# Optimization experiments

Measured on AMD Instinct MI355X. Metric: run time of the kernel, lower is better.

The kernel has to match this reference:

```python
import jax, jax.numpy as jnp
import numpy as np

B, N, C, H, NC, P = 16, 577, 768, 12, 8, 576  # batch, seq(=patches+cls), dim, heads, curves, patches
D = C // H


def setup_inputs() -> dict:
    key = jax.random.key(0)
    ks = jax.random.split(key, 8)
    x = jax.random.normal(ks[0], (B, N, C), jnp.float32)
    qkv_w = jax.random.normal(ks[1], (C, 3 * C), jnp.float32) * 0.02
    proj_w = jax.random.normal(ks[2], (C, C), jnp.float32) * 0.02
    proj_b = jnp.zeros((C,), jnp.float32)
    # learned per-head decay logits; +3 so sigmoid ~0.95 (slow decay, realistic)
    ai_list = jax.random.normal(ks[3], (NC, H), jnp.float32) + 3.0
    mask_weights = jax.random.normal(ks[4], (NC,), jnp.float32) * 0.1 + 1.0 / NC
    normalize = 1.0 + 0.1 * jax.random.normal(ks[5], (H,), jnp.float32)
    # space-filling-curve inverse index permutations (one per curve)
    curve_inds = jnp.stack([
        jax.random.permutation(jax.random.fold_in(ks[6], c), P) for c in range(NC)
    ]).astype(jnp.int32)
    return dict(x=x, qkv_w=qkv_w, proj_w=proj_w, proj_b=proj_b,
                ai_list=ai_list, mask_weights=mask_weights,
                normalize=normalize, curve_inds=curve_inds)


def _build_mask(ai_list, mask_weights, curve_inds):
    # sigmoid(a)^|i-j| gathered by the curve permutation == sigmoid(a)^|ind_i - ind_j|
    a = jax.nn.sigmoid(ai_list)                                  # [NC,H]
    ci = curve_inds.astype(jnp.float32)                          # [NC,P]
    diff = jnp.abs(ci[:, :, None] - ci[:, None, :])              # [NC,P,P]
    Mc = a[:, :, None, None] ** diff[:, None, :, :]              # [NC,H,P,P]
    Mp = jnp.einsum('c,chpq->hpq', mask_weights, Mc)             # weighted sum over curves
    # cls-token row/col: each curve contributes ones -> sum of weights
    sw = jnp.sum(mask_weights)
    M = jnp.pad(Mp, ((0, 0), (1, 0), (1, 0)))                    # [H,N,N]
    M = M.at[:, 0, :].set(sw)
    M = M.at[:, :, 0].set(sw)
    return M


def reference(x, qkv_w, proj_w, proj_b, ai_list, mask_weights, normalize, curve_inds):
    qkv = (x @ qkv_w).reshape(B, N, 3, H, D)
    q = jnp.transpose(qkv[:, :, 0], (0, 2, 1, 3))                # [B,H,N,D]
    k = jnp.transpose(qkv[:, :, 1], (0, 2, 1, 3))
    v = jnp.transpose(qkv[:, :, 2], (0, 2, 1, 3))
    # NOTE: original overwrites self.scale with the bool `scale`=True -> multiply by 1
    attn = jnp.einsum('bhnd,bhmd->bhnm', q, k)                   # [B,H,N,N]
    M = _build_mask(ai_list, mask_weights, curve_inds)           # [H,N,N]
    attn = attn * M[None] * normalize[None, :, None, None]       # method='mul_v1'
    attn = jax.nn.softmax(attn, axis=-1)
    out = jnp.einsum('bhnm,bhmd->bhnd', attn, v)
    out = jnp.transpose(out, (0, 2, 1, 3)).reshape(B, N, C)
    return out @ proj_w + proj_b
```

## Files before the change

kernel.cpp:

```cpp
#include <hip/hip_runtime.h>


typedef _Float16 f16;
typedef _Float16 half8 __attribute__((ext_vector_type(8)));
typedef _Float16 half4 __attribute__((ext_vector_type(4)));
typedef float floatx4 __attribute__((ext_vector_type(4)));

#define DEVINL __device__ __forceinline__

#define Bb 16
#define NN 577
#define CC 768
#define HH 12
#define DD 64
#define MM (Bb * NN)
#define VTLD 584
#define MLD 580
#define CLD 136

DEVINL void async_copy16(void* lds, const void* g) {
  __builtin_amdgcn_global_load_lds(
      (const __attribute__((address_space(1))) void*)g,
      (__attribute__((address_space(3))) void*)lds, 16, 0, 0);
}

DEVINL half8 ld_swz(const f16* lds, int row, int chunk) {
  return *(const half8*)(lds + row * 64 + ((chunk ^ (row & 7)) << 3));
}

DEVINL int xcd_swizzle(int orig, int nwg) {
  int q = nwg >> 3, r = nwg & 7;
  int xcd = orig & 7, loc = orig >> 3;
  return (xcd < r ? xcd * (q + 1) : r * (q + 1) + (xcd - r) * q) + loc;
}

__global__ void cvt_kernel(const float* __restrict__ in, f16* __restrict__ out, int n) {
  int i = (blockIdx.x * blockDim.x + threadIdx.x) * 4;
  if (i >= n) return;
  float4 v = *(const float4*)(in + i);
  half4 o = {(f16)v.x, (f16)v.y, (f16)v.z, (f16)v.w};
  *(half4*)(out + i) = o;
}

__global__ void transpose_cvt(const float* __restrict__ in, f16* __restrict__ out,
                              int N3, int K) {
  __shared__ float t[32][33];
  const int k0 = blockIdx.x * 32, n0 = blockIdx.y * 32;
  const int tx = threadIdx.x & 31, ty = threadIdx.x >> 5;
#pragma unroll
  for (int p = 0; p < 4; ++p)
    t[ty + p * 8][tx] = in[(size_t)(k0 + ty + p * 8) * N3 + n0 + tx];
  __syncthreads();
#pragma unroll
  for (int p = 0; p < 4; ++p)
    out[(size_t)(n0 + ty + p * 8) * K + k0 + tx] = (f16)t[tx][ty + p * 8];
}

__global__ void mask_kernel(const float* __restrict__ ai, const float* __restrict__ mw,
                            const float* __restrict__ nrm, const int* __restrict__ ci,
                            float* __restrict__ Mb) {
  const int i = blockIdx.x;
  const int h = blockIdx.y;
  __shared__ float la_s[8], wv_s[8], cif[8], swn_s;
  int tid = threadIdx.x;
  if (tid < 8) {
    float av = ai[tid * 12 + h];
    float a = 1.f / (1.f + __expf(-av));
    la_s[tid] = __logf(a);
    wv_s[tid] = mw[tid];
    cif[tid] = (i > 0) ? (float)ci[tid * 576 + (i - 1)] : 0.f;
  }
  if (tid == 0) {
    float s = 0.f;
    for (int c = 0; c < 8; ++c) s += mw[c];
    swn_s = s * nrm[h] * 1.44269504088896f;
  }
  __syncthreads();
  const float nr = nrm[h] * 1.44269504088896f;
  float* row = Mb + ((size_t)h * NN + i) * MLD;
  for (int j = tid; j < NN; j += blockDim.x) {
    float val;
    if (i == 0 || j == 0) {
      val = swn_s;
    } else {
      float acc = 0.f;
#pragma unroll
      for (int c = 0; c < 8; ++c) {
        float d = fabsf(cif[c] - (float)ci[c * 576 + (j - 1)]);
        acc += wv_s[c] * __expf(la_s[c] * d);
      }
      val = acc * nr;
    }
    row[j] = val;
  }
}

DEVINL void gemm_mainloop(const f16* __restrict__ A, const f16* __restrict__ Bt,
                          int K, int lda, int ldb, int arow0, int brow0, int maxar,
                          f16* As, f16* Bs, floatx4 acc[4][4], int tid) {
  const int lane = tid & 63;
  const int wid = tid >> 6;
  const int wr = wid >> 1, wc = wid & 1;
  const int l15 = lane & 15, g = lane >> 4;
  for (int k0 = 0; k0 < K; k0 += 64) {
#pragma unroll
    for (int q = 0; q < 4; ++q) {
      int idx = q * 256 + tid;
      int r = idx >> 3, cp = idx & 7;
      int lc = (cp ^ (r & 7)) << 3;
      int ar = arow0 + r; if (ar > maxar) ar = maxar;
      async_copy16(As + idx * 8, A + (size_t)ar * lda + k0 + lc);
      async_copy16(Bs + idx * 8, Bt + (size_t)(brow0 + r) * ldb + k0 + lc);
    }
    __syncthreads();
#pragma unroll
    for (int kk = 0; kk < 2; ++kk) {
      half8 af[4], bf[4];
#pragma unroll
      for (int mi = 0; mi < 4; ++mi) af[mi] = ld_swz(As, wr * 64 + mi * 16 + l15, kk * 4 + g);
#pragma unroll
      for (int ni = 0; ni < 4; ++ni) bf[ni] = ld_swz(Bs, wc * 64 + ni * 16 + l15, kk * 4 + g);
#pragma unroll
      for (int mi = 0; mi < 4; ++mi)
#pragma unroll
        for (int ni = 0; ni < 4; ++ni)
          acc[mi][ni] = __builtin_amdgcn_mfma_f32_16x16x32_f16(af[mi], bf[ni], acc[mi][ni], 0, 0, 0);
    }
    __syncthreads();
  }
}

__global__ __launch_bounds__(256, 3)
void gemm_qkv(const f16* __restrict__ A, const f16* __restrict__ Bt,
              f16* __restrict__ qb, f16* __restrict__ kb, f16* __restrict__ vt) {
  __shared__ __align__(16) f16 SMEM[128 * CLD];
  f16* As = SMEM;
  f16* Bs = SMEM + 8192;
  floatx4 acc[4][4] = {};
  const int nwg = 18 * 73;
  const int wgid = xcd_swizzle(blockIdx.y * gridDim.x + blockIdx.x, nwg);
  const int m0 = (wgid / 18) * 128, n0 = (wgid % 18) * 128;
  gemm_mainloop(A, Bt, CC, CC, CC, m0, n0, MM - 1, As, Bs, acc, threadIdx.x);
  const int tid = threadIdx.x, lane = tid & 63, wid = tid >> 6;
  const int wr = wid >> 1, wc = wid & 1, l15 = lane & 15, g = lane >> 4;
  const int t = n0 / CC;
  const int h0 = (n0 - t * CC) >> 6;
  if (t < 2) {
#pragma unroll
    for (int mi = 0; mi < 4; ++mi)
#pragma unroll
      for (int ni = 0; ni < 4; ++ni)
#pragma unroll
        for (int r = 0; r < 4; ++r)
          SMEM[(wr * 64 + mi * 16 + 4 * g + r) * CLD + wc * 64 + ni * 16 + l15] =
              (f16)acc[mi][ni][r];
    __syncthreads();
    f16* dst = (t == 0) ? qb : kb;
#pragma unroll
    for (int p = 0; p < 8; ++p) {
      int c = p * 256 + tid;
      int ml = c >> 4, n3c = (c & 15) << 3;
      int mg = m0 + ml;
      if (mg < MM) {
        int b = mg / NN, n = mg - b * NN;
        int h = h0 + (n3c >> 6), d0 = n3c & 63;
        half8 v = *(const half8*)(SMEM + ml * CLD + n3c);
        *(half8*)(dst + ((size_t)(b * HH + h) * NN + n) * DD + d0) = v;
      }
    }
  } else {
#pragma unroll
    for (int mi = 0; mi < 4; ++mi)
#pragma unroll
      for (int ni = 0; ni < 4; ++ni)
#pragma unroll
        for (int r = 0; r < 4; ++r)
          SMEM[(wc * 64 + ni * 16 + l15) * CLD + wr * 64 + mi * 16 + 4 * g + r] =
              (f16)acc[mi][ni][r];
    __syncthreads();
#pragma unroll
    for (int p = 0; p < 8; ++p) {
      int c = p * 256 + tid;
      int n3 = c >> 4, mc = (c & 15) << 3;
      int mg = m0 + mc;
      int h = h0 + (n3 >> 6), d = n3 & 63;
      half8 v = *(const half8*)(SMEM + n3 * CLD + mc);
      int b0 = mg / NN, b7 = (mg + 7) / NN;
      if (mg + 7 < MM && b0 == b7) {
        *(half8*)(vt + ((size_t)(b0 * HH + h) * DD + d) * VTLD + (mg - b0 * NN)) = v;
      } else {
#pragma unroll
        for (int e = 0; e < 8; ++e) {
          int m2 = mg + e;
          if (m2 < MM) {
            int b = m2 / NN;
            vt[((size_t)(b * HH + h) * DD + d) * VTLD + (m2 - b * NN)] = v[e];
          }
        }
      }
    }
  }
}

__global__ __launch_bounds__(256, 3)
void gemm_proj(const f16* __restrict__ A, const f16* __restrict__ Bt,
               const float* __restrict__ bias, float* __restrict__ out) {
  __shared__ f16 As[128 * 64], Bs[128 * 64];
  floatx4 acc[4][4] = {};
  const int nwg = 6 * 73;
  const int wgid = xcd_swizzle(blockIdx.y * gridDim.x + blockIdx.x, nwg);
  const int m0 = (wgid / 6) * 128, n0 = (wgid % 6) * 128;
  gemm_mainloop(A, Bt, CC, CC, CC, m0, n0, MM - 1, As, Bs, acc, threadIdx.x);
  const int lane = threadIdx.x & 63, wid = threadIdx.x >> 6;
  const int wr = wid >> 1, wc = wid & 1, l15 = lane & 15, g = lane >> 4;
#pragma unroll
  for (int mi = 0; mi < 4; ++mi)
#pragma unroll
    for (int ni = 0; ni < 4; ++ni)
#pragma unroll
      for (int r = 0; r < 4; ++r) {
        int m = m0 + wr * 64 + mi * 16 + 4 * g + r;
        if (m >= MM) continue;
        int n = n0 + wc * 64 + ni * 16 + l15;
        out[(size_t)m * CC + n] = acc[mi][ni][r] + bias[n];
      }
}

__global__ __launch_bounds__(256, 2)
void attn_kernel(const f16* __restrict__ qb, const f16* __restrict__ kb,
                 const f16* __restrict__ vt, const float* __restrict__ Mb,
                 f16* __restrict__ aout) {
  __shared__ f16 Ks[2][64 * 64];
  __shared__ f16 Vs[2][64 * 64];
  const int D0 = (blockIdx.z * gridDim.y + blockIdx.y) * gridDim.x + blockIdx.x;
  const int wgid = xcd_swizzle(D0, 5 * HH * Bb);
  const int it = wgid % 5;
  const int rem = wgid / 5;
  const int b = rem % Bb, h = rem / Bb;
  const int tid = threadIdx.x, lane = tid & 63, wid = tid >> 6;
  const int l15 = lane & 15, g = lane >> 4;
  const size_t bh = (size_t)b * HH + h;
  const f16* qbh = qb + bh * NN * DD;
  const f16* kbh = kb + bh * NN * DD;
  const f16* vbh = vt + bh * DD * VTLD;
  const float* Mh = Mb + (size_t)h * NN * MLD;
  const int row0w = it * 128 + wid * 32;

  half8 qB[2][2];
#pragma unroll
  for (int qt = 0; qt < 2; ++qt) {
    int qr = row0w + qt * 16 + l15; if (qr > NN - 1) qr = NN - 1;
    const f16* qp = qbh + (size_t)qr * DD + g * 8;
    qB[qt][0] = *(const half8*)qp;
    qB[qt][1] = *(const half8*)(qp + 32);
  }
  const float* Mrow0;
  const float* Mrow1;
  {
    int r0 = row0w + l15;      if (r0 > NN - 1) r0 = NN - 1;
    int r1 = row0w + 16 + l15; if (r1 > NN - 1) r1 = NN - 1;
    Mrow0 = Mh + (size_t)r0 * MLD + 4 * g;
    Mrow1 = Mh + (size_t)r1 * MLD + 4 * g;
  }

  floatx4 acc[2][4] = {};
  float lsum[2] = {0.f, 0.f};
  float mrun[2] = {-3e38f, -3e38f};

  auto stage = [&](f16* Kd, f16* Vd, int j0) {
#pragma unroll
    for (int qi = 0; qi < 2; ++qi) {
      int idx = qi * 256 + tid;
      int r = idx >> 3, cp = idx & 7;
      int lc = (cp ^ (r & 7)) << 3;
      int j = j0 + r; if (j > NN - 1) j = NN - 1;
      async_copy16(Kd + idx * 8, kbh + (size_t)j * DD + lc);
      async_copy16(Vd + idx * 8, vbh + (size_t)r * VTLD + j0 + lc);
    }
  };
  auto ldmask = [&](floatx4 m4[2][4], int j0) {
#pragma unroll
    for (int jt = 0; jt < 4; ++jt) {
      m4[0][jt] = *(const floatx4*)(Mrow0 + j0 + jt * 16);
      m4[1][jt] = *(const floatx4*)(Mrow1 + j0 + jt * 16);
    }
  };
  auto compute = [&](const f16* Kc, const f16* Vc, floatx4 m4[2][4], int j0) {
    floatx4 sf[2][4];
#pragma unroll
    for (int jt = 0; jt < 4; ++jt) {
      half8 ka0 = ld_swz(Kc, jt * 16 + l15, g);
      half8 ka1 = ld_swz(Kc, jt * 16 + l15, 4 + g);
#pragma unroll
      for (int qt = 0; qt < 2; ++qt) {
        floatx4 z = {0.f, 0.f, 0.f, 0.f};
        z = __builtin_amdgcn_mfma_f32_16x16x32_f16(ka0, qB[qt][0], z, 0, 0, 0);
        z = __builtin_amdgcn_mfma_f32_16x16x32_f16(ka1, qB[qt][1], z, 0, 0, 0);
        sf[qt][jt] = z;
      }
    }
    const bool tail = (j0 + 64 > NN);
    half4 pB[2][4];
#pragma unroll
    for (int qt = 0; qt < 2; ++qt) {
      float mx = mrun[qt];
#pragma unroll
      for (int jt = 0; jt < 4; ++jt)
#pragma unroll
        for (int r = 0; r < 4; ++r) {
          float s = sf[qt][jt][r] * m4[qt][jt][r];
          if (tail && (j0 + jt * 16 + 4 * g + r >= NN)) s = -3e38f;
          sf[qt][jt][r] = s;
          mx = fmaxf(mx, s);
        }
      mx = fmaxf(mx, __shfl_xor(mx, 16));
      mx = fmaxf(mx, __shfl_xor(mx, 32));
      float fac = __builtin_amdgcn_exp2f(mrun[qt] - mx);
      mrun[qt] = mx;
      lsum[qt] *= fac;
#pragma unroll
      for (int dt = 0; dt < 4; ++dt)
#pragma unroll
        for (int r = 0; r < 4; ++r) acc[qt][dt][r] *= fac;
      float ls = 0.f;
#pragma unroll
      for (int jt = 0; jt < 4; ++jt) {
        half4 pb;
#pragma unroll
        for (int r = 0; r < 4; ++r) {
          float p = __builtin_amdgcn_exp2f(sf[qt][jt][r] - mx);
          ls += p;
          pb[r] = (f16)p;
        }
        pB[qt][jt] = pb;
      }
      lsum[qt] += ls;
    }
#pragma unroll
    for (int dt = 0; dt < 4; ++dt)
#pragma unroll
      for (int jt = 0; jt < 4; ++jt) {
        int c16 = (jt * 2 + (g >> 1)) ^ (l15 & 7);
        half4 va = *(const half4*)(Vc + (dt * 16 + l15) * 64 + (c16 << 3) + (g & 1) * 4);
#pragma unroll
        for (int qt = 0; qt < 2; ++qt)
          acc[qt][dt] = __builtin_amdgcn_mfma_f32_16x16x16f16(va, pB[qt][jt], acc[qt][dt], 0, 0, 0);
      }
  };

  floatx4 m4A[2][4], m4B[2][4];
  stage(Ks[0], Vs[0], 0);
  ldmask(m4A, 0);

#pragma unroll 1
  for (int t = 0; t < 10; t += 2) {
    ldmask(m4B, (t + 1) * 64);
    asm volatile("s_waitcnt vmcnt(8)" ::: "memory");
    __builtin_amdgcn_s_barrier();
    __builtin_amdgcn_sched_barrier(0);
    stage(Ks[1], Vs[1], (t + 1) * 64);
    compute(Ks[0], Vs[0], m4A, t * 64);
    const int j2 = (t + 2 < 10) ? (t + 2) * 64 : 0;
    ldmask(m4A, j2);
    asm volatile("s_waitcnt vmcnt(8)" ::: "memory");
    __builtin_amdgcn_s_barrier();
    __builtin_amdgcn_sched_barrier(0);
    stage(Ks[0], Vs[0], j2);
    compute(Ks[1], Vs[1], m4B, (t + 1) * 64);
  }

#pragma unroll
  for (int qt = 0; qt < 2; ++qt) {
    float v = lsum[qt];
    v += __shfl_xor(v, 16);
    v += __shfl_xor(v, 32);
    float linv = 1.f / v;
    int n = row0w + qt * 16 + l15;
    if (n < NN) {
#pragma unroll
      for (int dt = 0; dt < 4; ++dt) {
        half4 o;
#pragma unroll
        for (int r = 0; r < 4; ++r) o[r] = (f16)(acc[qt][dt][r] * linv);
        *(half4*)(aout + ((size_t)(b * NN + n)) * CC + h * DD + dt * 16 + 4 * g) = o;
      }
    }
  }
}

extern "C" void kernel_launch(void* const* d_in, const int* in_sizes, int n_in,
                              void* d_out, int out_size, void* d_ws, size_t ws_size,
                              hipStream_t stream) {
  const float* x    = (const float*)d_in[0];
  const float* qkvw = (const float*)d_in[1];
  const float* pw   = (const float*)d_in[2];
  const float* pb   = (const float*)d_in[3];
  const float* ai   = (const float*)d_in[4];
  const float* mw   = (const float*)d_in[5];
  const float* nrm  = (const float*)d_in[6];
  const int*   ci   = (const int*)d_in[7];
  float* out = (float*)d_out;

  char* wsb = (char*)d_ws;
  size_t off = 0;
  auto alloc = [&](size_t bytes) {
    char* p = wsb + off;
    off += (bytes + 255) & ~(size_t)255;
    return p;
  };
  f16*   x_h  = (f16*)alloc((size_t)MM * CC * 2);
  f16*   w_t  = (f16*)alloc((size_t)3 * CC * CC * 2);
  f16*   pw_t = (f16*)alloc((size_t)CC * CC * 2);
  float* Mb   = (float*)alloc((size_t)HH * NN * MLD * 4 + 1024);
  f16*   qb   = (f16*)alloc((size_t)Bb * HH * NN * DD * 2);
  f16*   kb   = (f16*)alloc((size_t)Bb * HH * NN * DD * 2);
  f16*   vt   = (f16*)alloc((size_t)Bb * HH * DD * VTLD * 2);
  (void)alloc(4096);
  f16* aout = x_h;

  cvt_kernel<<<(MM * CC / 4 + 255) / 256, 256, 0, stream>>>(x, x_h, MM * CC);
  transpose_cvt<<<dim3(CC / 32, 3 * CC / 32), 256, 0, stream>>>(qkvw, w_t, 3 * CC, CC);
  transpose_cvt<<<dim3(CC / 32, CC / 32), 256, 0, stream>>>(pw, pw_t, CC, CC);
  mask_kernel<<<dim3(NN, HH), 256, 0, stream>>>(ai, mw, nrm, ci, Mb);
  gemm_qkv<<<dim3(18, 73), 256, 0, stream>>>(x_h, w_t, qb, kb, vt);
  attn_kernel<<<dim3(5, HH, Bb), 256, 0, stream>>>(qb, kb, vt, Mb, aout);
  gemm_proj<<<dim3(6, 73), 256, 0, stream>>>(aout, pw_t, pb, out);
}
```

Measured before the change: 163.8 us.

## Skip online-softmax rescale for small max growth and raise attention occupancy

Result: slower. 229.7 us (+40.2%).

```diff
diff --git a/kernel.cpp b/kernel.cpp
--- a/kernel.cpp
+++ b/kernel.cpp
@@ -226,7 +226,7 @@
       }
 }
 
-__global__ __launch_bounds__(256, 2)
+__global__ __launch_bounds__(256, 3)
 void attn_kernel(const f16* __restrict__ qb, const f16* __restrict__ kb,
                  const f16* __restrict__ vt, const float* __restrict__ Mb,
                  f16* __restrict__ aout) {
@@ -299,42 +299,55 @@
         sf[qt][jt] = z;
       }
     }
-    const bool tail = (j0 + 64 > NN);
+#pragma unroll
+    for (int qt = 0; qt < 2; ++qt)
+#pragma unroll
+      for (int jt = 0; jt < 4; ++jt)
+#pragma unroll
+        for (int r = 0; r < 4; ++r) sf[qt][jt][r] *= m4[qt][jt][r];
+    if (j0 + 64 > NN) {
+#pragma unroll
+      for (int qt = 0; qt < 2; ++qt)
+#pragma unroll
+        for (int jt = 0; jt < 4; ++jt)
+#pragma unroll
+          for (int r = 0; r < 4; ++r)
+            if (j0 + jt * 16 + 4 * g + r >= NN) sf[qt][jt][r] = -3e38f;
+    }
     half4 pB[2][4];
 #pragma unroll
     for (int qt = 0; qt < 2; ++qt) {
-      float mx = mrun[qt];
+      float pj[4];
 #pragma unroll
       for (int jt = 0; jt < 4; ++jt)
-#pragma unroll
-        for (int r = 0; r < 4; ++r) {
-          float s = sf[qt][jt][r] * m4[qt][jt][r];
-          if (tail && (j0 + jt * 16 + 4 * g + r >= NN)) s = -3e38f;
-          sf[qt][jt][r] = s;
-          mx = fmaxf(mx, s);
-        }
-      mx = fmaxf(mx, __shfl_xor(mx, 16));
-      mx = fmaxf(mx, __shfl_xor(mx, 32));
-      float fac = __builtin_amdgcn_exp2f(mrun[qt] - mx);
-      mrun[qt] = mx;
-      lsum[qt] *= fac;
-#pragma unroll
-      for (int dt = 0; dt < 4; ++dt)
-#pragma unroll
-        for (int r = 0; r < 4; ++r) acc[qt][dt][r] *= fac;
-      float ls = 0.f;
+        pj[jt] = fmaxf(fmaxf(sf[qt][jt][0], sf[qt][jt][1]),
+                       fmaxf(sf[qt][jt][2], sf[qt][jt][3]));
+      float pmax = fmaxf(fmaxf(pj[0], pj[1]), fmaxf(pj[2], pj[3]));
+      pmax = fmaxf(pmax, __shfl_xor(pmax, 16));
+      pmax = fmaxf(pmax, __shfl_xor(pmax, 32));
+      if (!__all(pmax - mrun[qt] <= 8.f)) {
+        float mnew = fmaxf(mrun[qt], pmax);
+        float fac = __builtin_amdgcn_exp2f(mrun[qt] - mnew);
+        mrun[qt] = mnew;
+        lsum[qt] *= fac;
+#pragma unroll
+        for (int dt = 0; dt < 4; ++dt)
+#pragma unroll
+          for (int r = 0; r < 4; ++r) acc[qt][dt][r] *= fac;
+      }
+      float lsj[4];
 #pragma unroll
       for (int jt = 0; jt < 4; ++jt) {
         half4 pb;
-#pragma unroll
-        for (int r = 0; r < 4; ++r) {
-          float p = __builtin_amdgcn_exp2f(sf[qt][jt][r] - mx);
-          ls += p;
-          pb[r] = (f16)p;
-        }
+        float p0 = __builtin_amdgcn_exp2f(sf[qt][jt][0] - mrun[qt]);
+        float p1 = __builtin_amdgcn_exp2f(sf[qt][jt][1] - mrun[qt]);
+        float p2 = __builtin_amdgcn_exp2f(sf[qt][jt][2] - mrun[qt]);
+        float p3 = __builtin_amdgcn_exp2f(sf[qt][jt][3] - mrun[qt]);
+        pb[0] = (f16)p0; pb[1] = (f16)p1; pb[2] = (f16)p2; pb[3] = (f16)p3;
+        lsj[jt] = (p0 + p1) + (p2 + p3);
         pB[qt][jt] = pb;
       }
-      lsum[qt] += ls;
+      lsum[qt] += (lsj[0] + lsj[1]) + (lsj[2] + lsj[3]);
     }
 #pragma unroll
     for (int dt = 0; dt < 4; ++dt)
```
